# Optimization experiments

Measured on AMD Instinct MI355X. Metric: run time of the kernel, lower is better.

The kernel has to match this reference:

```python
import jax
import jax.numpy as jnp
import numpy as np
from jax import lax

B, NS, T, H, V = 4, 96, 8, 256, 32000
L = NS * T
N = NS + 1                    # num_nodes = num_statements + 1 (exit node)
NUM_LAYERS = NS // 16         # avg_statements_per_step = 16 -> 6 execution steps


def _lstm(c, h, x, Wx, Wh, b):
    """flax-style LSTM cell: gates in (i, f, g, o) order."""
    z = x @ Wx + h @ Wh + b
    gi, gf, gg, go = jnp.split(z, 4, axis=-1)
    c2 = jax.nn.sigmoid(gf) * c + jax.nn.sigmoid(gi) * jnp.tanh(gg)
    h2 = jax.nn.sigmoid(go) * jnp.tanh(c2)
    return c2, h2


def _forward(code_statements, code_length, embed, Wx_s, Wh_s, b_s, W_se, b_se,
             Wx_e, Wh_e, b_e, W_hk, b_hk, W_sd, b_sd, W_d1, b_d1, init_a, init_b):
    # ---- statement embedding: LSTM over the T tokens of each statement ----
    tok = embed[code_statements.astype(jnp.int32)]            # [B, L, H]
    tok = jnp.transpose(tok.reshape(B * NS, T, H), (1, 0, 2))  # [T, B*NS, H]
    c0 = jnp.zeros((B * NS, H), tok.dtype)

    def scan_fn(carry, x):
        c, hh = carry
        c, hh = _lstm(c, hh, x, Wx_s, Wh_s, b_s)
        return (c, hh), None

    (_, h_last), _ = lax.scan(scan_fn, (c0, c0), tok)
    stmt = h_last.reshape(B, NS, H)                           # [B, NS, H]

    # ---- skip encoder: pairwise segment-sum embedding for skipping i -> j ----
    node = jnp.concatenate([stmt, jnp.zeros((B, 1, H), stmt.dtype)], axis=1)  # [B,N,H]
    pref = jnp.concatenate(
        [jnp.zeros((B, 1, H), stmt.dtype), jnp.cumsum(node, axis=1)], axis=1)[:, :N]
    skip = (pref[:, None, :, :] - pref[:, :, None, :]) @ W_se + b_se  # [B,N,N,H]

    stmt_len = (code_length // T).astype(jnp.int32)           # exit node index per example

    # ---- execution loop with soft instruction pointer ----
    c = jnp.broadcast_to(init_a, (B, N, H))
    h = jnp.broadcast_to(init_b, (B, N, H))
    p = jnp.zeros((B, N)).at[:, 0].set(1.0)

    def step(c, h, p, skip_nnh, length, layer):
        # per-example: c,h [N,H]; p [N]; skip_nnh [N,N,H]; length scalar
        n = p.shape[0]
        ar = jnp.arange(n)
        if layer == 0:
            mask = jnp.zeros((n, n)).at[:, 1].set(1.0)
        elif layer == NUM_LAYERS - 1:
            mask = jnp.zeros((n, n)).at[:, length].set(1.0)   # force skip to exit
        else:
            mask = 1.0 - jnp.tri(n)                           # strictly forward skips
            mask = jnp.where(ar <= length, mask, 0.0)         # no skips past exit
            mask = mask.at[:, length].set(1.0)                # always allow exit

        # skip attention logits
        skip_keys = skip_nnh @ W_sd + b_sd                    # [N,N,H]
        h_key = h @ W_hk + b_hk                               # [N,H]
        act = jax.nn.relu(jnp.concatenate(
            [jnp.broadcast_to(h_key[:, None, :], (n, n, H)), skip_keys], axis=-1))
        skip_logits = jnp.squeeze(act @ W_d1, -1) + b_d1[0]   # [N,N]
        skip_logits = jnp.where(mask > 0, skip_logits, -jnp.inf)
        skip_p = jax.nn.softmax(skip_logits, axis=-1)

        # one LSTM skip-execution step for every (i, j) pair, vectorized
        z = skip_nnh @ Wx_e + (h @ Wh_e)[:, None, :] + b_e    # [N,N,4H]
        gi, gf, gg, go = jnp.split(z, 4, axis=-1)
        c_prop = jax.nn.sigmoid(gf) * c[:, None, :] + jax.nn.sigmoid(gi) * jnp.tanh(gg)
        h_prop = jax.nn.sigmoid(go) * jnp.tanh(c_prop)
        fwd_edge = (ar[None, :] > ar[:, None])[:, :, None]    # only j > i executes
        c_prop = jnp.where(fwd_edge, c_prop, c[:, None, :])
        h_prop = jnp.where(fwd_edge, h_prop, h[:, None, :])
        valid = (mask[:, :, None] > 0) & (p[:, None, None] > 0)
        c_prop = jnp.where(valid, c_prop, 0.0)
        h_prop = jnp.where(valid, h_prop, 0.0)

        # soft aggregation of proposals weighted by p(i) * skip_p(i -> j)
        w = skip_p * p[:, None]                               # [N,N]
        denom = (w.sum(axis=0) + 1e-7)[:, None]               # [N,1]
        c_new = jnp.einsum('ijh,ij->jh', c_prop, w) / denom
        h_new = jnp.einsum('ijh,ij->jh', h_prop, w) / denom
        p_new = p @ skip_p
        return c_new, h_new, p_new

    for layer in range(NUM_LAYERS):
        c, h, p = jax.vmap(step, in_axes=(0, 0, 0, 0, 0, None))(
            c, h, p, skip, stmt_len, layer)
    return h                                                  # [B, N, H]


def setup_inputs() -> dict:
    key = jax.random.key(0)
    ks = jax.random.split(key, 16)

    def dense(k, fi, fo):
        return jax.random.normal(k, (fi, fo)) * (1.0 / np.sqrt(fi))

    return {
        'code_statements': jax.random.randint(ks[0], (B, L), 0, V, dtype=jnp.int32),
        'code_length': jax.random.randint(ks[1], (B,), 64, L, dtype=jnp.int32),
        'embed': jax.random.normal(ks[2], (V, H)) * 0.02,
        'Wx_s': dense(ks[3], H, 4 * H), 'Wh_s': dense(ks[4], H, 4 * H),
        'b_s': jnp.zeros((4 * H,)),
        'W_se': dense(ks[5], H, H), 'b_se': jnp.zeros((H,)),
        'Wx_e': dense(ks[6], H, 4 * H), 'Wh_e': dense(ks[7], H, 4 * H),
        'b_e': jnp.zeros((4 * H,)),
        'W_hk': dense(ks[8], H, H), 'b_hk': jnp.zeros((H,)),
        'W_sd': dense(ks[9], H, H), 'b_sd': jnp.zeros((H,)),
        'W_d1': dense(ks[10], 2 * H, 1), 'b_d1': jnp.zeros((1,)),
        'init_a': jax.random.normal(ks[11], (H,)),
        'init_b': jax.random.normal(ks[12], (H,)),
    }


def reference(code_statements, code_length, embed, Wx_s, Wh_s, b_s, W_se, b_se,
              Wx_e, Wh_e, b_e, W_hk, b_hk, W_sd, b_sd, W_d1, b_d1, init_a, init_b):
    return _forward(code_statements, code_length, embed, Wx_s, Wh_s, b_s, W_se, b_se,
                    Wx_e, Wh_e, b_e, W_hk, b_hk, W_sd, b_sd, W_d1, b_d1, init_a, init_b)
```

## Files before the change

kernel.cpp:

```cpp
#include <hip/hip_runtime.h>
#include <cstddef>

#define B_   4
#define NS_  96
#define T_   8
#define H_   256
#define N_   97
#define NL_  6
#define R_   388

__device__ __forceinline__ float sigm(float x) {
    return __builtin_amdgcn_rcpf(1.0f + __builtin_amdgcn_exp2f(-1.44269504f * x));
}
__device__ __forceinline__ float tanh_f(float x) {
    return 1.0f - 2.0f * __builtin_amdgcn_rcpf(1.0f + __builtin_amdgcn_exp2f(2.88539008f * x));
}

__device__ __forceinline__ void fma16(float4 a, float4 w0, float4 w1, float4 w2,
                                      float4 w3, float* acc) {
    acc[0] = fmaf(a.x, w0.x, acc[0]); acc[1] = fmaf(a.x, w0.y, acc[1]);
    acc[2] = fmaf(a.x, w0.z, acc[2]); acc[3] = fmaf(a.x, w0.w, acc[3]);
    acc[0] = fmaf(a.y, w1.x, acc[0]); acc[1] = fmaf(a.y, w1.y, acc[1]);
    acc[2] = fmaf(a.y, w1.z, acc[2]); acc[3] = fmaf(a.y, w1.w, acc[3]);
    acc[0] = fmaf(a.z, w2.x, acc[0]); acc[1] = fmaf(a.z, w2.y, acc[1]);
    acc[2] = fmaf(a.z, w2.z, acc[2]); acc[3] = fmaf(a.z, w2.w, acc[3]);
    acc[0] = fmaf(a.w, w3.x, acc[0]); acc[1] = fmaf(a.w, w3.y, acc[1]);
    acc[2] = fmaf(a.w, w3.z, acc[2]); acc[3] = fmaf(a.w, w3.w, acc[3]);
}

__global__ __launch_bounds__(512, 4) void prologue(
        const int* __restrict__ ids, const float* __restrict__ embed,
        const float* __restrict__ Wx_s, const float* __restrict__ b_s,
        const float* __restrict__ b_se, const float* __restrict__ Wx_e,
        const float* __restrict__ b_e, const float* __restrict__ W_sd,
        const float* __restrict__ b_sd, const float* __restrict__ Wh_e,
        const float* __restrict__ init_a, const float* __restrict__ init_b,
        float* __restrict__ xz, float* __restrict__ cz, float* __restrict__ ck,
        float* __restrict__ hw, float* __restrict__ c0, float* __restrict__ h0,
        float* __restrict__ p0) {
    int bid = blockIdx.x, t = threadIdx.x;
    if (bid < 384) {
        __shared__ float As[64][260];
        __shared__ int ridx[64];
        int r0 = (bid >> 3) * 64, n0 = (bid & 7) * 128;
        if (t < 64) ridx[t] = ids[r0 + t];
        __syncthreads();
#pragma unroll
        for (int m = 0; m < 8; m++) {
            int L = m * 512 + t;
            int r = L >> 6, c4 = (L & 63) * 4;
            *(float4*)&As[r][c4] = *(const float4*)(embed + (size_t)ridx[r] * 256 + c4);
        }
        __syncthreads();
        int rg = t >> 5, cg = t & 31;
        float acc[4][4] = {};
        const float* wp = Wx_s + n0 + 4 * cg;
#pragma unroll 4
        for (int kb = 0; kb < 64; kb++) {
            float4 w0 = *(const float4*)(wp + (size_t)(4 * kb + 0) * 1024);
            float4 w1 = *(const float4*)(wp + (size_t)(4 * kb + 1) * 1024);
            float4 w2 = *(const float4*)(wp + (size_t)(4 * kb + 2) * 1024);
            float4 w3 = *(const float4*)(wp + (size_t)(4 * kb + 3) * 1024);
#pragma unroll
            for (int i = 0; i < 4; i++) {
                float4 a = *(const float4*)&As[rg * 4 + i][4 * kb];
                fma16(a, w0, w1, w2, w3, acc[i]);
            }
        }
        int col = n0 + 4 * cg;
        float4 bv = *(const float4*)&b_s[col];
#pragma unroll
        for (int i = 0; i < 4; i++) {
            int r = r0 + rg * 4 + i;
            float4 o = make_float4(acc[i][0] + bv.x, acc[i][1] + bv.y,
                                   acc[i][2] + bv.z, acc[i][3] + bv.w);
            *(float4*)&xz[(size_t)r * 1024 + col] = o;
        }
    } else if (bid < 386) {
        int n = (bid - 384) * 512 + t;
        float acc = b_e[n];
        for (int k = 0; k < 256; k++) acc = fmaf(b_se[k], Wx_e[(size_t)k * 1024 + n], acc);
        cz[n] = acc;
    } else if (bid < 388) {
        int n = (bid - 386) * 512 + t;
        float acc = b_e[n];
        for (int k = 0; k < 256; k++) {
            acc = fmaf(b_se[k], Wx_e[(size_t)k * 1024 + n], acc);
            acc = fmaf(init_b[k], Wh_e[(size_t)k * 1024 + n], acc);
        }
        hw[n] = acc;
    } else if (bid == 388) {
        if (t < 256) {
            float acc = b_sd[t];
            for (int k = 0; k < 256; k++) acc = fmaf(b_se[k], W_sd[(size_t)k * 256 + t], acc);
            ck[t] = acc;
        }
    } else {
        int r0 = (bid - 389) * 8 + (t >> 8) * 4;
        int col = t & 255;
        float ia = init_a[col], ib = init_b[col];
#pragma unroll
        for (int rr = 0; rr < 4; rr++) {
            int row = r0 + rr;
            if (row < R_) {
                c0[(size_t)row * 256 + col] = ia;
                h0[(size_t)row * 256 + col] = ib;
                if (col == 0) p0[row] = ((row % N_) == 0) ? 1.0f : 0.0f;
            }
        }
    }
}

__global__ __launch_bounds__(1024, 4) void lstm_onepass(const float* __restrict__ xz,
        const float* __restrict__ Wh, float* __restrict__ hbuf) {
    __shared__ float zpart[4][4][1024];
    __shared__ float h_s[4][260];
    int t = threadIdx.x;
    int s0 = blockIdx.x * 4;
    int kg = t >> 8, tg = t & 255;
    int sg = t >> 8, cc = t & 255;
    float creg;
    float hreg;
    {
        const float* z0 = xz + ((size_t)(s0 + sg) * T_) * 1024;
        float gi = z0[cc], gg = z0[512 + cc], go = z0[768 + cc];
        creg = sigm(gi) * tanh_f(gg);
        hreg = sigm(go) * tanh_f(creg);
        h_s[sg][cc] = hreg;
    }
    __syncthreads();
    for (int step = 1; step < T_; step++) {
        float4 z[4] = {};
        const float* wp = Wh + (size_t)(kg * 64) * 1024 + 4 * tg;
        int kbase = kg * 64;
#pragma unroll 4
        for (int kb = 0; kb < 16; kb++) {
            float4 w0 = *(const float4*)(wp + (size_t)(4 * kb + 0) * 1024);
            float4 w1 = *(const float4*)(wp + (size_t)(4 * kb + 1) * 1024);
            float4 w2 = *(const float4*)(wp + (size_t)(4 * kb + 2) * 1024);
            float4 w3 = *(const float4*)(wp + (size_t)(4 * kb + 3) * 1024);
            int k = kbase + 4 * kb;
#pragma unroll
            for (int s = 0; s < 4; s++) {
                float4 a = *(const float4*)&h_s[s][k];
                fma16(a, w0, w1, w2, w3, (float*)&z[s]);
            }
        }
#pragma unroll
        for (int s = 0; s < 4; s++)
            *(float4*)&zpart[kg][s][4 * tg] = z[s];
        __syncthreads();
        const float* xzp = xz + ((size_t)(s0 + sg) * T_ + step) * 1024;
        float zv[4];
#pragma unroll
        for (int ga = 0; ga < 4; ga++) {
            int zc = ga * 256 + cc;
            zv[ga] = xzp[zc] + zpart[0][sg][zc] + zpart[1][sg][zc]
                   + zpart[2][sg][zc] + zpart[3][sg][zc];
        }
        creg = sigm(zv[1]) * creg + sigm(zv[0]) * tanh_f(zv[2]);
        hreg = sigm(zv[3]) * tanh_f(creg);
        h_s[sg][cc] = hreg;
        __syncthreads();
    }
    hbuf[(size_t)(s0 + sg) * H_ + cc] = hreg;
}

template<int MT>
__global__ __launch_bounds__(256) void gemm_t(const float* __restrict__ A,
        const float* __restrict__ W, const float* __restrict__ bias,
        const float* __restrict__ subQ, const float* __restrict__ pgate,
        float* __restrict__ C, int R, int NC) {
    __shared__ float As[MT][260];
    __shared__ int anyflag;
    int t = threadIdx.x;
    int n0 = blockIdx.x * 128;
    int r0 = blockIdx.y * MT;
    if (pgate) {
        if (t == 0) anyflag = 0;
        __syncthreads();
        if (t < MT && r0 + t < R && pgate[r0 + t] != 0.0f) anyflag = 1;
        __syncthreads();
        if (!anyflag) return;
    }
#pragma unroll
    for (int m = 0; m < MT / 4; m++) {
        int L = m * 256 + t;
        int r = L >> 6, c4 = (L & 63) * 4;
        int rr = r0 + r;
        float4 v = make_float4(0.f, 0.f, 0.f, 0.f);
        if (rr < R) v = *(const float4*)(A + (size_t)rr * 256 + c4);
        *(float4*)&As[r][c4] = v;
    }
    __syncthreads();
    constexpr int RT = MT / 8;
    int rg = t >> 5, cg = t & 31;
    float acc[RT][4] = {};
    const float* wp = W + n0 + 4 * cg;
#pragma unroll 2
    for (int kb = 0; kb < 64; kb++) {
        float4 w0 = *(const float4*)(wp + (size_t)(4 * kb + 0) * NC);
        float4 w1 = *(const float4*)(wp + (size_t)(4 * kb + 1) * NC);
        float4 w2 = *(const float4*)(wp + (size_t)(4 * kb + 2) * NC);
        float4 w3 = *(const float4*)(wp + (size_t)(4 * kb + 3) * NC);
#pragma unroll
        for (int i = 0; i < RT; i++) {
            float4 a = *(const float4*)&As[rg * RT + i][4 * kb];
            fma16(a, w0, w1, w2, w3, acc[i]);
        }
    }
    int col = n0 + 4 * cg;
    float4 bv = make_float4(0.f, 0.f, 0.f, 0.f);
    if (bias) bv = *(const float4*)&bias[col];
#pragma unroll
    for (int i = 0; i < RT; i++) {
        int r = r0 + rg * RT + i;
        if (r < R) {
            float4 o = make_float4(acc[i][0] + bv.x, acc[i][1] + bv.y,
                                   acc[i][2] + bv.z, acc[i][3] + bv.w);
            if (subQ) {
                float4 s4 = *(const float4*)(subQ + (size_t)r * NC + col);
                o.x -= s4.x; o.y -= s4.y; o.z -= s4.z; o.w -= s4.w;
            }
            *(float4*)&C[(size_t)r * NC + col] = o;
        }
    }
}

__global__ __launch_bounds__(256) void qr_kernel(const float* __restrict__ S,
        const float* __restrict__ Wx_e, const float* __restrict__ W_sd,
        const float* __restrict__ hw, float* __restrict__ q, float* __restrict__ ve0,
        float* __restrict__ r_, float* __restrict__ rT) {
    __shared__ float As[16][260];
    int t = threadIdx.x;
    int bx = blockIdx.x;
    int r0 = blockIdx.y * 16;
#pragma unroll
    for (int m = 0; m < 4; m++) {
        int L = m * 256 + t;
        int r = L >> 6, c4 = (L & 63) * 4;
        int rr = r0 + r;
        float4 v = make_float4(0.f, 0.f, 0.f, 0.f);
        if (rr < R_) v = *(const float4*)(S + (size_t)rr * 256 + c4);
        *(float4*)&As[r][c4] = v;
    }
    __syncthreads();
    bool isq = bx < 8;
    const float* W = isq ? Wx_e : W_sd;
    int NC = isq ? 1024 : 256;
    int n0 = (isq ? bx : bx - 8) * 128;
    int rg = t >> 5, cg = t & 31;
    float acc[2][4] = {};
    const float* wp = W + n0 + 4 * cg;
#pragma unroll 2
    for (int kb = 0; kb < 64; kb++) {
        float4 w0 = *(const float4*)(wp + (size_t)(4 * kb + 0) * NC);
        float4 w1 = *(const float4*)(wp + (size_t)(4 * kb + 1) * NC);
        float4 w2 = *(const float4*)(wp + (size_t)(4 * kb + 2) * NC);
        float4 w3 = *(const float4*)(wp + (size_t)(4 * kb + 3) * NC);
#pragma unroll
        for (int i = 0; i < 2; i++) {
            float4 a = *(const float4*)&As[rg * 2 + i][4 * kb];
            fma16(a, w0, w1, w2, w3, acc[i]);
        }
    }
    int col = n0 + 4 * cg;
#pragma unroll
    for (int i = 0; i < 2; i++) {
        int r = r0 + rg * 2 + i;
        if (r < R_) {
            float4 o = make_float4(acc[i][0], acc[i][1], acc[i][2], acc[i][3]);
            if (isq) {
                *(float4*)&q[(size_t)r * 1024 + col] = o;
                float4 hwv = *(const float4*)&hw[col];
                float4 v0 = make_float4(hwv.x - o.x, hwv.y - o.y, hwv.z - o.z, hwv.w - o.w);
                *(float4*)&ve0[(size_t)r * 1024 + col] = v0;
            } else {
                *(float4*)&r_[(size_t)r * 256 + col] = o;
                int b = r / N_, n = r - b * N_;
                rT[((size_t)b * 256 + col + 0) * 128 + n] = o.x;
                rT[((size_t)b * 256 + col + 1) * 128 + n] = o.y;
                rT[((size_t)b * 256 + col + 2) * 128 + n] = o.z;
                rT[((size_t)b * 256 + col + 3) * 128 + n] = o.w;
            }
        }
    }
}

__global__ __launch_bounds__(1024) void cumsum_k(const float* __restrict__ stmt,
                                                 float* __restrict__ pref) {
    __shared__ float buf[96][256];
    int b = blockIdx.x, t = threadIdx.x;
#pragma unroll
    for (int m = 0; m < 6; m++) {
        int L = m * 1024 + t;
        int r = L >> 6, c4 = (L & 63) * 4;
        *(float4*)&buf[r][c4] = *(const float4*)(stmt + ((size_t)b * NS_ + r) * 256 + c4);
    }
    __syncthreads();
    if (t < 256) {
        float run = 0.0f;
        pref[((size_t)b * N_) * H_ + t] = 0.0f;
        for (int n = 1; n < N_; n++) {
            run += buf[n - 1][t];
            pref[((size_t)b * N_ + n) * H_ + t] = run;
        }
    }
}

__global__ void softmax_once(const float* __restrict__ r, const float* __restrict__ rT,
                             const float* __restrict__ ck, const float* __restrict__ Wd1,
                             const int* __restrict__ code_length,
                             float* __restrict__ spT_mid, float* __restrict__ spT0,
                             float* __restrict__ spT5) {
    __shared__ float ri[H_], ckl[H_], wd[H_];
    __shared__ float part[8][128];
    __shared__ float red[4];
    int t = threadIdx.x;
    int j = t & 127, half = t >> 7;
    int bi = blockIdx.x;
    int b = bi / N_, i = bi % N_;
    if (t < H_) {
        ri[t] = r[(size_t)bi * H_ + t];
        ckl[t] = ck[t];
        wd[t] = Wd1[256 + t];
    }
    __syncthreads();
    int len = code_length[b] / T_;
    bool valid = (j < N_) && ((j > i && j <= len) || (j == len));
    float acc = 0.0f;
    if (valid) {
        const float* rTb = rT + (size_t)b * H_ * 128 + j;
        int h0 = half * 32;
#pragma unroll 4
        for (int hh = 0; hh < 32; hh++) {
            int h = h0 + hh;
            float v = rTb[(size_t)h * 128] - ri[h] + ckl[h];
            acc = fmaf(fmaxf(v, 0.0f), wd[h], acc);
        }
    }
    part[half][j] = acc;
    __syncthreads();
    float logit = -3.0e38f;
    if (t < 128) {
        if (valid)
            logit = part[0][j] + part[1][j] + part[2][j] + part[3][j]
                  + part[4][j] + part[5][j] + part[6][j] + part[7][j];
        float m = logit;
#pragma unroll
        for (int off = 32; off; off >>= 1) m = fmaxf(m, __shfl_xor(m, off));
        if ((t & 63) == 0) red[t >> 6] = m;
    }
    __syncthreads();
    float e = 0.0f;
    if (t < 128) {
        float m = fmaxf(red[0], red[1]);
        e = valid ? __builtin_amdgcn_exp2f(1.44269504f * (logit - m)) : 0.0f;
        float s = e;
#pragma unroll
        for (int off = 32; off; off >>= 1) s += __shfl_xor(s, off);
        if ((t & 63) == 0) red[2 + (t >> 6)] = s;
    }
    __syncthreads();
    if (t < 128 && j < N_) {
        float s = red[2] + red[3];
        size_t o = ((size_t)b * N_ + j) * 128 + i;
        spT_mid[o] = e / s;
        spT0[o] = (j == 1) ? 1.0f : 0.0f;
        spT5[o] = (j == len) ? 1.0f : 0.0f;
    }
}

__global__ __launch_bounds__(512) void aggregate(const float* __restrict__ q,
        const float* __restrict__ ve, const float* __restrict__ spT,
        const float* __restrict__ p, const float* __restrict__ cc,
        const float* __restrict__ hc, float* __restrict__ cn,
        float* __restrict__ hn, float* __restrict__ pn) {
    __shared__ float qj[1024];
    __shared__ float wcol[128];
    __shared__ int vlist[128];
    __shared__ int cnts[2];
    __shared__ float wsums[2];
    __shared__ float parts[2][2][H_];
    int t = threadIdx.x;
    int bj = blockIdx.x;
    int b = bj / N_, j = bj - b * N_;
    bool pred = false;
    int rank = 0;
    if (t < 128) {
        float wv = (t < N_) ? spT[(size_t)bj * 128 + t] * p[b * N_ + t] : 0.f;
        wcol[t] = wv;
        float s = wv;
#pragma unroll
        for (int off = 32; off; off >>= 1) s += __shfl_xor(s, off);
        pred = (wv != 0.0f);
        unsigned long long mask = __ballot(pred);
        int lane = t & 63;
        rank = __popcll(mask & ((1ull << lane) - 1ull));
        if (lane == 0) { cnts[t >> 6] = (int)__popcll(mask); wsums[t >> 6] = s; }
    }
    __syncthreads();
    float wsum = wsums[0] + wsums[1];
    int nv = cnts[0] + cnts[1];
    if (t < 128 && pred) vlist[(t >= 64 ? cnts[0] : 0) + rank] = t;
    if (wsum == 0.0f) {
        if (t < 256) {
            cn[(size_t)bj * H_ + t] = 0.0f;
            hn[(size_t)bj * H_ + t] = 0.0f;
            if (t == 0) pn[bj] = 0.0f;
        }
        return;
    }
    qj[t] = q[(size_t)bj * 1024 + t];
    qj[512 + t] = q[(size_t)bj * 1024 + 512 + t];
    __syncthreads();
    int hh = t & 255, vs = t >> 8;
    float ac = 0.f, ah = 0.f;
    for (int v = vs; v < nv; v += 2) {
        int i = vlist[v];
        float wv = wcol[i];
        size_t rowi = (size_t)b * N_ + i;
        if (j > i) {
            const float* vei = ve + rowi * 1024;
            float gi = qj[hh] + vei[hh];
            float gf = qj[256 + hh] + vei[256 + hh];
            float gg = qj[512 + hh] + vei[512 + hh];
            float go = qj[768 + hh] + vei[768 + hh];
            float c2 = cc[rowi * H_ + hh];
            float cp = sigm(gf) * c2 + sigm(gi) * tanh_f(gg);
            float hp = sigm(go) * tanh_f(cp);
            ac = fmaf(wv, cp, ac);
            ah = fmaf(wv, hp, ah);
        } else {
            ac = fmaf(wv, cc[rowi * H_ + hh], ac);
            ah = fmaf(wv, hc[rowi * H_ + hh], ah);
        }
    }
    parts[vs][0][hh] = ac;
    parts[vs][1][hh] = ah;
    __syncthreads();
    if (t < 256) {
        float inv = __builtin_amdgcn_rcpf(wsum + 1e-7f);
        cn[(size_t)bj * H_ + t] = (parts[0][0][t] + parts[1][0][t]) * inv;
        hn[(size_t)bj * H_ + t] = (parts[0][1][t] + parts[1][1][t]) * inv;
        if (t == 0) pn[bj] = wsum;
    }
}


extern "C" void kernel_launch(void* const* d_in, const int* in_sizes, int n_in,
                              void* d_out, int out_size, void* d_ws, size_t ws_size,
                              hipStream_t stream) {
    const int*   code_statements = (const int*)d_in[0];
    const int*   code_length = (const int*)d_in[1];
    const float* embed = (const float*)d_in[2];
    const float* Wx_s = (const float*)d_in[3];
    const float* Wh_s = (const float*)d_in[4];
    const float* b_s  = (const float*)d_in[5];
    const float* W_se = (const float*)d_in[6];
    const float* b_se = (const float*)d_in[7];
    const float* Wx_e = (const float*)d_in[8];
    const float* Wh_e = (const float*)d_in[9];
    const float* b_e  = (const float*)d_in[10];
    const float* W_sd = (const float*)d_in[13];
    const float* b_sd = (const float*)d_in[14];
    const float* W_d1 = (const float*)d_in[15];
    const float* init_a = (const float*)d_in[17];
    const float* init_b = (const float*)d_in[18];
    float* out = (float*)d_out;

    float* wsf = (float*)d_ws;
    size_t off = 0;
    auto alloc = [&](size_t n) { float* p = wsf + off; off += n; return p; };
    float* cz = alloc(1024);
    float* ck = alloc(256);
    float* hw = alloc(1024);
    float* xz = alloc((size_t)3072 * 1024);
    float* stmt = alloc(384 * 256);
    float* pref = alloc(R_ * 256);
    float* s_   = alloc(R_ * 256);
    float* q  = alloc(R_ * 1024);
    float* r_ = alloc(R_ * 256);
    float* rT = alloc(4 * 256 * 128);
    float* ve = alloc(R_ * 1024);
    float* spT_mid = alloc(R_ * 128);
    float* spT0    = alloc(R_ * 128);
    float* spT5    = alloc(R_ * 128);
    float* p0 = alloc(R_);
    float* p1 = alloc(R_);
    float* c0 = alloc(R_ * 256);
    float* c1 = alloc(R_ * 256);
    float* h0 = alloc(R_ * 256);
    float* h1 = alloc(R_ * 256);

    prologue<<<dim3(438), 512, 0, stream>>>(code_statements, embed, Wx_s, b_s,
                                            b_se, Wx_e, b_e, W_sd, b_sd, Wh_e,
                                            init_a, init_b, xz, cz, ck, hw, c0, h0, p0);
    lstm_onepass<<<dim3(96), 1024, 0, stream>>>(xz, Wh_s, stmt);
    cumsum_k<<<dim3(4), 1024, 0, stream>>>(stmt, pref);
    gemm_t<16><<<dim3(2, 25), 256, 0, stream>>>(pref, W_se, nullptr, nullptr, nullptr,
                                                s_, R_, 256);
    qr_kernel<<<dim3(10, 25), 256, 0, stream>>>(s_, Wx_e, W_sd, hw, q, ve, r_, rT);
    softmax_once<<<dim3(R_), 1024, 0, stream>>>(r_, rT, ck, W_d1, code_length,
                                                spT_mid, spT0, spT5);

    for (int layer = 0; layer < NL_; layer++) {
        bool odd = (layer & 1);
        float* pc = odd ? p1 : p0;
        float* pn = odd ? p0 : p1;
        float* cc = odd ? c1 : c0;
        float* cn = odd ? c0 : c1;
        float* hc = odd ? h1 : h0;
        float* hn = odd ? h0 : h1;
        if (layer == NL_ - 1) hn = out;
        const float* spT = (layer == 0) ? spT0 : (layer == NL_ - 1) ? spT5 : spT_mid;
        aggregate<<<dim3(R_), 512, 0, stream>>>(q, ve, spT, pc, cc, hc, cn, hn, pn);
        if (layer < NL_ - 1)
            gemm_t<16><<<dim3(8, 25), 256, 0, stream>>>(hn, Wh_e, cz, q, pn,
                                                        ve, R_, 1024);
    }
}
```

Before: 371.5 us.

## Halve statements per LSTM block and cache part of Wh in LDS

The statement LSTM kernel now handles 2 sequences per block instead of 4, doubling the grid to 192 blocks so more of the GPU's compute units are busy. Each block stages the first 28 rows of Wh in shared memory, which cuts part of the per-step global weight reads for the first k-group, and prefetches the xz inputs before the recurrent matmul. The cost is that every block now streams Wh itself, so total weight traffic roughly doubles. Half the threads also sit idle during the gate update, and the k-group split becomes uneven.

```diff
diff --git a/kernel.cpp b/kernel.cpp
--- a/kernel.cpp
+++ b/kernel.cpp
@@ -111,17 +111,23 @@
     }
 }
 
-__global__ __launch_bounds__(1024, 4) void lstm_onepass(const float* __restrict__ xz,
+__global__ __launch_bounds__(1024) void lstm_onepass(const float* __restrict__ xz,
         const float* __restrict__ Wh, float* __restrict__ hbuf) {
-    __shared__ float zpart[4][4][1024];
-    __shared__ float h_s[4][260];
+    __shared__ float zpart[4][2][1024];
+    __shared__ float h_s[2][260];
+    __shared__ float Wh_c[28][1024];
     int t = threadIdx.x;
-    int s0 = blockIdx.x * 4;
+    int s0 = blockIdx.x * 2;
     int kg = t >> 8, tg = t & 255;
-    int sg = t >> 8, cc = t & 255;
-    float creg;
-    float hreg;
-    {
+    int sg = (t >> 8) & 1, cc = t & 255;
+#pragma unroll
+    for (int m = 0; m < 7; m++) {
+        int L = m * 1024 + t;
+        int r = L >> 8, c4 = (L & 255) * 4;
+        *(float4*)&Wh_c[r][c4] = *(const float4*)(Wh + (size_t)r * 1024 + c4);
+    }
+    float creg = 0.0f, hreg = 0.0f;
+    if (t < 512) {
         const float* z0 = xz + ((size_t)(s0 + sg) * T_) * 1024;
         float gi = z0[cc], gg = z0[512 + cc], go = z0[768 + cc];
         creg = sigm(gi) * tanh_f(gg);
@@ -130,40 +136,76 @@
     }
     __syncthreads();
     for (int step = 1; step < T_; step++) {
-        float4 z[4] = {};
+        float x0 = 0.f, x1 = 0.f, x2 = 0.f, x3 = 0.f;
+        if (t < 512) {
+            const float* xzp = xz + ((size_t)(s0 + sg) * T_ + step) * 1024;
+            x0 = xzp[cc]; x1 = xzp[256 + cc]; x2 = xzp[512 + cc]; x3 = xzp[768 + cc];
+        }
+        float4 z[2] = {};
         const float* wp = Wh + (size_t)(kg * 64) * 1024 + 4 * tg;
         int kbase = kg * 64;
+        if (kg == 0) {
+#pragma unroll
+            for (int kb = 0; kb < 7; kb++) {
+                float4 w0 = *(const float4*)&Wh_c[4 * kb + 0][4 * tg];
+                float4 w1 = *(const float4*)&Wh_c[4 * kb + 1][4 * tg];
+                float4 w2 = *(const float4*)&Wh_c[4 * kb + 2][4 * tg];
+                float4 w3 = *(const float4*)&Wh_c[4 * kb + 3][4 * tg];
+                int k = 4 * kb;
+#pragma unroll
+                for (int s = 0; s < 2; s++) {
+                    float4 a = *(const float4*)&h_s[s][k];
+                    fma16(a, w0, w1, w2, w3, (float*)&z[s]);
+                }
+            }
+#pragma unroll 3
+            for (int kb = 7; kb < 16; kb++) {
+                float4 w0 = *(const float4*)(wp + (size_t)(4 * kb + 0) * 1024);
+                float4 w1 = *(const float4*)(wp + (size_t)(4 * kb + 1) * 1024);
+                float4 w2 = *(const float4*)(wp + (size_t)(4 * kb + 2) * 1024);
+                float4 w3 = *(const float4*)(wp + (size_t)(4 * kb + 3) * 1024);
+                int k = 4 * kb;
+#pragma unroll
+                for (int s = 0; s < 2; s++) {
+                    float4 a = *(const float4*)&h_s[s][k];
+                    fma16(a, w0, w1, w2, w3, (float*)&z[s]);
+                }
+            }
+        } else {
 #pragma unroll 4
-        for (int kb = 0; kb < 16; kb++) {
-            float4 w0 = *(const float4*)(wp + (size_t)(4 * kb + 0) * 1024);
-            float4 w1 = *(const float4*)(wp + (size_t)(4 * kb + 1) * 1024);
-            float4 w2 = *(const float4*)(wp + (size_t)(4 * kb + 2) * 1024);
-            float4 w3 = *(const float4*)(wp + (size_t)(4 * kb + 3) * 1024);
-            int k = kbase + 4 * kb;
-#pragma unroll
-            for (int s = 0; s < 4; s++) {
-                float4 a = *(const float4*)&h_s[s][k];
-                fma16(a, w0, w1, w2, w3, (float*)&z[s]);
-            }
-        }
-#pragma unroll
-        for (int s = 0; s < 4; s++)
+            for (int kb = 0; kb < 16; kb++) {
+                float4 w0 = *(const float4*)(wp + (size_t)(4 * kb + 0) * 1024);
+                float4 w1 = *(const float4*)(wp + (size_t)(4 * kb + 1) * 1024);
+                float4 w2 = *(const float4*)(wp + (size_t)(4 * kb + 2) * 1024);
+                float4 w3 = *(const float4*)(wp + (size_t)(4 * kb + 3) * 1024);
+                int k = kbase + 4 * kb;
+#pragma unroll
+                for (int s = 0; s < 2; s++) {
+                    float4 a = *(const float4*)&h_s[s][k];
+                    fma16(a, w0, w1, w2, w3, (float*)&z[s]);
+                }
+            }
+        }
+#pragma unroll
+        for (int s = 0; s < 2; s++)
             *(float4*)&zpart[kg][s][4 * tg] = z[s];
         __syncthreads();
-        const float* xzp = xz + ((size_t)(s0 + sg) * T_ + step) * 1024;
-        float zv[4];
-#pragma unroll
-        for (int ga = 0; ga < 4; ga++) {
-            int zc = ga * 256 + cc;
-            zv[ga] = xzp[zc] + zpart[0][sg][zc] + zpart[1][sg][zc]
-                   + zpart[2][sg][zc] + zpart[3][sg][zc];
-        }
-        creg = sigm(zv[1]) * creg + sigm(zv[0]) * tanh_f(zv[2]);
-        hreg = sigm(zv[3]) * tanh_f(creg);
-        h_s[sg][cc] = hreg;
+        if (t < 512) {
+            float zv0 = x0 + zpart[0][sg][cc] + zpart[1][sg][cc]
+                      + zpart[2][sg][cc] + zpart[3][sg][cc];
+            float zv1 = x1 + zpart[0][sg][256 + cc] + zpart[1][sg][256 + cc]
+                      + zpart[2][sg][256 + cc] + zpart[3][sg][256 + cc];
+            float zv2 = x2 + zpart[0][sg][512 + cc] + zpart[1][sg][512 + cc]
+                      + zpart[2][sg][512 + cc] + zpart[3][sg][512 + cc];
+            float zv3 = x3 + zpart[0][sg][768 + cc] + zpart[1][sg][768 + cc]
+                      + zpart[2][sg][768 + cc] + zpart[3][sg][768 + cc];
+            creg = sigm(zv1) * creg + sigm(zv0) * tanh_f(zv2);
+            hreg = sigm(zv3) * tanh_f(creg);
+            h_s[sg][cc] = hreg;
+        }
         __syncthreads();
     }
-    hbuf[(size_t)(s0 + sg) * H_ + cc] = hreg;
+    if (t < 512) hbuf[(size_t)(s0 + sg) * H_ + cc] = hreg;
 }
 
 template<int MT>
@@ -496,7 +538,7 @@
     prologue<<<dim3(438), 512, 0, stream>>>(code_statements, embed, Wx_s, b_s,
                                             b_se, Wx_e, b_e, W_sd, b_sd, Wh_e,
                                             init_a, init_b, xz, cz, ck, hw, c0, h0, p0);
-    lstm_onepass<<<dim3(96), 1024, 0, stream>>>(xz, Wh_s, stmt);
+    lstm_onepass<<<dim3(192), 1024, 0, stream>>>(xz, Wh_s, stmt);
     cumsum_k<<<dim3(4), 1024, 0, stream>>>(stmt, pref);
     gemm_t<16><<<dim3(2, 25), 256, 0, stream>>>(pref, W_se, nullptr, nullptr, nullptr,
                                                 s_, R_, 256);
```

New measurement: 372.5 us. Within noise of the previous version (+0.3%).
